# Optimization experiments

Measured on AMD Instinct MI355X. Metric: run time of the kernel, lower is better.

The kernel has to match this reference:

```python
import jax, jax.numpy as jnp
import numpy as np

RHO = 0.5
SIGMA = 0.3
BATCH = 32768
L = 1024

# Concrete drifts (abstract in the original base class): classic linear filtering pair
# b(x, y) = -x  (mean-reverting state drift), B(x, y) = x (observation drift = state)
def _b(x, y):
    return -x

def _B(x, y):
    return x


def setup_inputs() -> dict:
    key = jax.random.key(0)
    k1, k2, k3 = jax.random.split(key, 3)
    x0 = jax.random.normal(k1, (BATCH,), dtype=jnp.float32)
    y0 = jax.random.normal(k2, (BATCH,), dtype=jnp.float32)
    ts = (jnp.arange(L, dtype=jnp.float32) / (L - 1))  # uniform grid on [0, 1]
    z = jax.random.normal(k3, (L - 1, BATCH, 2), dtype=jnp.float32)
    return {"x0": x0, "y0": y0, "ts": ts, "z": z}


def reference(x0, y0, ts, z):
    hs = ts[1:] - ts[:-1]  # (L-1,)

    def step(carry, inp):
        x, y = carry
        h, zi = inp  # h scalar, zi (batch, 2)
        sqrt_h = jnp.sqrt(h)
        dW1 = sqrt_h * zi[:, 1]
        # faithful to source: dW[:,0] = rho^2*dW[:,0] + (1-rho^2)*dW[:,1]
        dW0 = RHO ** 2 * (sqrt_h * zi[:, 0]) + (1.0 - RHO ** 2) * dW1
        x_new = x + _b(x, y) * h + SIGMA * dW0
        # note: source updates x first, then uses the NEW x inside B
        y_new = y + _B(x_new, y) * h + dW1
        return (x_new, y_new), jnp.stack((x_new, y_new), axis=1)  # (batch, 2)

    (_, _), traj = jax.lax.scan(step, (x0, y0), (hs, z))  # traj: (L-1, batch, 2)
    xy0 = jnp.stack((x0, y0), axis=1)[None]  # (1, batch, 2)
    xy = jnp.concatenate([xy0, traj], axis=0)  # (L, batch, 2)
    return jnp.transpose(xy, (1, 0, 2))  # (batch, L, 2)
```

## Files before the change

kernel.cpp:

```cpp
#include <hip/hip_runtime.h>

#define BATCH 32768
#define LEN   1024
#define TT    16
#define NTK   64
#define WV    8
#define PB    128

typedef float f32x4 __attribute__((ext_vector_type(4)));


#define BAR() do { asm volatile("s_waitcnt lgkmcnt(0)" ::: "memory"); \
                   __builtin_amdgcn_s_barrier(); } while (0)

#define STEP(ZI) do { \
    xa = fmaf(xa, q, fmaf(Ax, ZI.x, Bx * ZI.y)); \
    ya = ya + fmaf(xa, h, sh * ZI.y); \
    xb = fmaf(xb, q, fmaf(Ax, ZI.z, Bx * ZI.w)); \
    yb = yb + fmaf(xb, h, sh * ZI.w); \
} while (0)

#define ROUND(R, CUR, NXT, PRE_, FIRST_) do { \
    const int k_ = 8 * (R) + w - off; \
    if (PRE_) {   \
        const int kn_ = 8 * ((R) + 1) + w - off;    \
        if ((unsigned)kn_ < (unsigned)NTK) { \
            const int rowb_ = 16 * kn_ - 1; \
            _Pragma("unroll") \
            for (int j = 0; j < TT; ++j) \
                NXT[j] = zb4[(size_t)(rowb_ + j) << 14]; \
        } \
    } \
    if ((unsigned)k_ < (unsigned)NTK) { \
        float xa, ya, xb, yb; \
        if (FIRST_ && k_ == 0) { xa = xi.x; ya = yi.x; xb = xi.y; yb = yi.y; } \
        else                   { xa = 0.f;  ya = 0.f;  xb = 0.f;  yb = 0.f;  } \
        float* tb0_ = ttile + ((size_t)w * PB + 2 * lane) * 36; \
        _Pragma("unroll") \
        for (int j = 0; j < TT; j += 2) { \
            float2 pa0_, pb0_; \
            if (FIRST_ && k_ == 0 && j == 0) { \
                pa0_ = make_float2(xa, ya); pb0_ = make_float2(xb, yb); \
            } else { \
                const float4 zi_ = CUR[j]; STEP(zi_); \
                pa0_ = make_float2(xa, ya); pb0_ = make_float2(xb, yb); \
            } \
            const float4 zi1_ = CUR[j + 1]; STEP(zi1_); \
            const int o_ = 4 * ((j >> 1) ^ csw); \
            *(float4*)&tb0_[o_]      = make_float4(pa0_.x, pa0_.y, xa, ya); \
            *(float4*)&tb0_[36 + o_] = make_float4(pb0_.x, pb0_.y, xb, yb); \
        } \
        *(float4*)&arr[w][4 * lane] = make_float4(xa, ya, xb, yb); \
    } \
    BAR();   \
    if (w == 0) { \
        _Pragma("unroll") \
        for (int wp = 0; wp < WV; ++wp) { \
            const int kp_ = 8 * (R) + wp - off; \
            if ((unsigned)kp_ < (unsigned)NTK) { \
                const float4 s_ = *(const float4*)&arr[wp][4 * lane]; \
                *(float4*)&arr[wp][4 * lane] = make_float4(U0, V0, U1, V1); \
                const float nU0_ = fmaf(ALPHA, U0, s_.x); \
                V0 = s_.y + V0 + GAL * U0;  U0 = nU0_; \
                const float nU1_ = fmaf(ALPHA, U1, s_.z); \
                V1 = s_.w + V1 + GAL * U1;  U1 = nU1_; \
            } \
        } \
    } \
    BAR();   \
    { \
        const int kw_ = 8 * (R) + wt - off; \
        if ((unsigned)kw_ < (unsigned)NTK) { \
            const int colf_ = (8 * (R) - off) * 32 + 4 * lane; \
            _Pragma("unroll") \
            for (int i = 0; i < 16; ++i) { \
                const int p_ = w * 16 + i; \
                const float4 t_ = *(const float4*)&ttile[ \
                    ((size_t)wt * PB + p_) * 36 + 4 * (csw ^ ((p_ >> 1) & 7))]; \
                const float2 uv_ = *(const float2*)&arr[wt][2 * p_]; \
                f32x4 o_; \
                o_.x = fmaf(uv_.x, a0, t_.x); \
                o_.y = t_.y + uv_.y + uv_.x * g0; \
                o_.z = fmaf(uv_.x, a1, t_.z); \
                o_.w = t_.w + uv_.y + uv_.x * g1; \
                __builtin_nontemporal_store(o_, \
                    (f32x4*)&out[(size_t)(bb + p_) * 2048 + colf_]); \
            } \
        } \
    } \
    BAR();   \
} while (0)

__global__ __launch_bounds__(512, 2)
void sde_kernel(const float* __restrict__ x0,
                const float* __restrict__ y0,
                const float* __restrict__ ts,
                const float* __restrict__ z,
                float* __restrict__ out)
{
    const int tid  = threadIdx.x;
    const int lane = tid & 63;
    const int w    = tid >> 6;
    const int bb   = blockIdx.x * PB;

    __shared__ __align__(16) float ttile[WV * PB * 36];
    __shared__ __align__(16) float arr[WV][260];

    const float h  = (ts[LEN - 1] - ts[0]) * (1.0f / 1023.0f);
    const float q  = 1.0f - h;
    const float sh = sqrtf(h);
    const float Ax = 0.075f * sh;
    const float Bx = 0.225f * sh;
    const float q2 = q * q, q4 = q2 * q2, q8 = q4 * q4;
    const float ALPHA = q8 * q8;
    const float GAL   = q * (1.0f - ALPHA);

    const int off = blockIdx.x & 7;

    const float2 xi = *(const float2*)&x0[bb + 2 * lane];
    const float2 yi = *(const float2*)&y0[bb + 2 * lane];

    const int   csw  = lane & 7;
    const int   jloc = (2 * lane) & 15;
    const float a0 = exp2f((float)(jloc + 1) * log2f(q));
    const float a1 = a0 * q;
    const float g0 = q * (1.0f - a0);
    const float g1 = q * (1.0f - a1);
    const int   wt = lane >> 3;

    const float4* zb4 = (const float4*)z + (bb >> 1) + lane;

    float U0 = 0.f, V0 = 0.f, U1 = 0.f, V1 = 0.f;

    float4 zvA[TT], zvB[TT];

    {
        const int k0 = w - off;
        if ((unsigned)k0 < (unsigned)NTK) {
            const int rowb = 16 * k0 - 1;
#pragma unroll
            for (int j = 0; j < TT; ++j) {
                int row = rowb + j;
                row = row < 0 ? 0 : row;
                zvA[j] = zb4[(size_t)row << 14];
            }
        }
    }

    ROUND(0, zvA, zvB, 1, 1);
    ROUND(1, zvB, zvA, 1, 0);
    ROUND(2, zvA, zvB, 1, 0);
    ROUND(3, zvB, zvA, 1, 0);
    ROUND(4, zvA, zvB, 1, 0);
    ROUND(5, zvB, zvA, 1, 0);
    ROUND(6, zvA, zvB, 1, 0);
    ROUND(7, zvB, zvA, 1, 0);
    ROUND(8, zvA, zvB, 0, 0);
}

extern "C" void kernel_launch(void* const* d_in, const int* in_sizes, int n_in,
                              void* d_out, int out_size, void* d_ws, size_t ws_size,
                              hipStream_t stream) {
    const float* x0 = (const float*)d_in[0];
    const float* y0 = (const float*)d_in[1];
    const float* ts = (const float*)d_in[2];
    const float* z  = (const float*)d_in[3];
    float* out = (float*)d_out;
    (void)d_ws; (void)ws_size; (void)in_sizes; (void)n_in; (void)out_size;

    sde_kernel<<<BATCH / PB, 512, 0, stream>>>(x0, y0, ts, z, out);
}
```

Measured before the change: 92.22 us.

## Process one path per lane with 64-path blocks to raise occupancy

Each lane now simulates a single batch path instead of two, so blocks cover 64 paths instead of 128. The z prefetch buffers shrink from float4 to float2, the scan carries and LDS tiles are halved, and launch bounds ask for 4 blocks per CU instead of 2. The writeback loop is re-indexed so each lane still writes a contiguous float4 of the output. The goal is more waves in flight to hide global latency, at the cost of 8-byte rather than 16-byte z loads per lane and twice as many blocks, each paying the same barrier and combine overhead.

Measured after the change: 116.5 us. 1.26x slower.

```diff
diff --git a/kernel.cpp b/kernel.cpp
--- a/kernel.cpp
+++ b/kernel.cpp
@@ -5,7 +5,8 @@
 #define TT    16
 #define NTK   64
 #define WV    8
-#define PB    128
+#define PB    64
+#define TS    36
 
 typedef float f32x4 __attribute__((ext_vector_type(4)));
 
@@ -14,10 +15,8 @@
                    __builtin_amdgcn_s_barrier(); } while (0)
 
 #define STEP(ZI) do { \
-    xa = fmaf(xa, q, fmaf(Ax, ZI.x, Bx * ZI.y)); \
-    ya = ya + fmaf(xa, h, sh * ZI.y); \
-    xb = fmaf(xb, q, fmaf(Ax, ZI.z, Bx * ZI.w)); \
-    yb = yb + fmaf(xb, h, sh * ZI.w); \
+    x = fmaf(x, q, fmaf(Ax, ZI.x, Bx * ZI.y)); \
+    y = y + fmaf(x, h, sh * ZI.y); \
 } while (0)
 
 #define ROUND(R, CUR, NXT, PRE_, FIRST_) do { \
@@ -28,29 +27,27 @@
             const int rowb_ = 16 * kn_ - 1; \
             _Pragma("unroll") \
             for (int j = 0; j < TT; ++j) \
-                NXT[j] = zb4[(size_t)(rowb_ + j) << 14]; \
+                NXT[j] = zb2[(size_t)(rowb_ + j) * BATCH]; \
         } \
     } \
     if ((unsigned)k_ < (unsigned)NTK) { \
-        float xa, ya, xb, yb; \
-        if (FIRST_ && k_ == 0) { xa = xi.x; ya = yi.x; xb = xi.y; yb = yi.y; } \
-        else                   { xa = 0.f;  ya = 0.f;  xb = 0.f;  yb = 0.f;  } \
-        float* tb0_ = ttile + ((size_t)w * PB + 2 * lane) * 36; \
+        float x, y; \
+        if (FIRST_ && k_ == 0) { x = xiv; y = yiv; } \
+        else                   { x = 0.f; y = 0.f; } \
+        float* tb_ = ttile + (w * PB + lane) * TS; \
         _Pragma("unroll") \
         for (int j = 0; j < TT; j += 2) { \
-            float2 pa0_, pb0_; \
+            float2 p0_; \
             if (FIRST_ && k_ == 0 && j == 0) { \
-                pa0_ = make_float2(xa, ya); pb0_ = make_float2(xb, yb); \
+                p0_ = make_float2(x, y);             \
             } else { \
-                const float4 zi_ = CUR[j]; STEP(zi_); \
-                pa0_ = make_float2(xa, ya); pb0_ = make_float2(xb, yb); \
+                const float2 z0_ = CUR[j]; STEP(z0_); \
+                p0_ = make_float2(x, y); \
             } \
-            const float4 zi1_ = CUR[j + 1]; STEP(zi1_); \
-            const int o_ = 4 * ((j >> 1) ^ csw); \
-            *(float4*)&tb0_[o_]      = make_float4(pa0_.x, pa0_.y, xa, ya); \
-            *(float4*)&tb0_[36 + o_] = make_float4(pb0_.x, pb0_.y, xb, yb); \
+            const float2 z1_ = CUR[j + 1]; STEP(z1_); \
+            *(float4*)&tb_[4 * ((j >> 1) ^ csw)] = make_float4(p0_.x, p0_.y, x, y); \
         } \
-        *(float4*)&arr[w][4 * lane] = make_float4(xa, ya, xb, yb); \
+        arr[w][lane] = make_float2(x, y);            \
     } \
     BAR();   \
     if (w == 0) { \
@@ -58,40 +55,38 @@
         for (int wp = 0; wp < WV; ++wp) { \
             const int kp_ = 8 * (R) + wp - off; \
             if ((unsigned)kp_ < (unsigned)NTK) { \
-                const float4 s_ = *(const float4*)&arr[wp][4 * lane]; \
-                *(float4*)&arr[wp][4 * lane] = make_float4(U0, V0, U1, V1); \
-                const float nU0_ = fmaf(ALPHA, U0, s_.x); \
-                V0 = s_.y + V0 + GAL * U0;  U0 = nU0_; \
-                const float nU1_ = fmaf(ALPHA, U1, s_.z); \
-                V1 = s_.w + V1 + GAL * U1;  U1 = nU1_; \
+                const float2 s_ = arr[wp][lane]; \
+                arr[wp][lane] = make_float2(U, V);   \
+                const float nU_ = fmaf(ALPHA, U, s_.x); \
+                V = s_.y + V + GAL * U;  U = nU_; \
             } \
         } \
     } \
     BAR();   \
     { \
-        const int kw_ = 8 * (R) + wt - off; \
+        const int kw_ = 8 * (R) + wl - off;          \
         if ((unsigned)kw_ < (unsigned)NTK) { \
-            const int colf_ = (8 * (R) - off) * 32 + 4 * lane; \
+            const int colf_ = (8 * (R) - off) * 32 + 32 * wl + 4 * sl; \
             _Pragma("unroll") \
-            for (int i = 0; i < 16; ++i) { \
-                const int p_ = w * 16 + i; \
+            for (int i = 0; i < 8; ++i) { \
+                const int row_ = w * 8 + i; \
                 const float4 t_ = *(const float4*)&ttile[ \
-                    ((size_t)wt * PB + p_) * 36 + 4 * (csw ^ ((p_ >> 1) & 7))]; \
-                const float2 uv_ = *(const float2*)&arr[wt][2 * p_]; \
+                    (wl * PB + row_) * TS + 4 * (sl ^ (row_ & 7))]; \
+                const float2 uv_ = arr[wl][row_]; \
                 f32x4 o_; \
                 o_.x = fmaf(uv_.x, a0, t_.x); \
                 o_.y = t_.y + uv_.y + uv_.x * g0; \
                 o_.z = fmaf(uv_.x, a1, t_.z); \
                 o_.w = t_.w + uv_.y + uv_.x * g1; \
                 __builtin_nontemporal_store(o_, \
-                    (f32x4*)&out[(size_t)(bb + p_) * 2048 + colf_]); \
+                    (f32x4*)&out[(size_t)(bb + row_) * 2048 + colf_]); \
             } \
         } \
     } \
     BAR();   \
 } while (0)
 
-__global__ __launch_bounds__(512, 2)
+__global__ __launch_bounds__(512, 4)
 void sde_kernel(const float* __restrict__ x0,
                 const float* __restrict__ y0,
                 const float* __restrict__ ts,
@@ -103,8 +98,8 @@
     const int w    = tid >> 6;
     const int bb   = blockIdx.x * PB;
 
-    __shared__ __align__(16) float ttile[WV * PB * 36];
-    __shared__ __align__(16) float arr[WV][260];
+    __shared__ __align__(16) float  ttile[WV * PB * TS];
+    __shared__ __align__(16) float2 arr[WV][66];
 
     const float h  = (ts[LEN - 1] - ts[0]) * (1.0f / 1023.0f);
     const float q  = 1.0f - h;
@@ -117,22 +112,22 @@
 
     const int off = blockIdx.x & 7;
 
-    const float2 xi = *(const float2*)&x0[bb + 2 * lane];
-    const float2 yi = *(const float2*)&y0[bb + 2 * lane];
+    const float xiv = x0[bb + lane];
+    const float yiv = y0[bb + lane];
 
-    const int   csw  = lane & 7;
-    const int   jloc = (2 * lane) & 15;
-    const float a0 = exp2f((float)(jloc + 1) * log2f(q));
+    const int   csw = lane & 7;
+    const int   wl  = lane >> 3;
+    const int   sl  = lane & 7;
+    const float a0 = exp2f((float)(2 * sl + 1) * log2f(q));
     const float a1 = a0 * q;
     const float g0 = q * (1.0f - a0);
     const float g1 = q * (1.0f - a1);
-    const int   wt = lane >> 3;
 
-    const float4* zb4 = (const float4*)z + (bb >> 1) + lane;
+    const float2* zb2 = (const float2*)z + bb + lane;
 
-    float U0 = 0.f, V0 = 0.f, U1 = 0.f, V1 = 0.f;
+    float U = 0.f, V = 0.f;
 
-    float4 zvA[TT], zvB[TT];
+    float2 zvA[TT], zvB[TT];
 
     {
         const int k0 = w - off;
@@ -142,7 +137,7 @@
             for (int j = 0; j < TT; ++j) {
                 int row = rowb + j;
                 row = row < 0 ? 0 : row;
-                zvA[j] = zb4[(size_t)row << 14];
+                zvA[j] = zb2[(size_t)row * BATCH];
             }
         }
     }
```
